# Kernel optimization log

Hardware: AMD Instinct MI355X
Metric: run time of the kernel (lower is better)

The kernel has to match this reference:

```python
import jax, jax.numpy as jnp
import numpy as np

B, T, D_IN, H1, H2 = 1024, 512, 128, 100, 100


def setup_inputs() -> dict:
    key = jax.random.key(0)
    ks = jax.random.split(key, 9)
    s1 = 1.0 / np.sqrt(H1)  # PyTorch LSTMCell init scale
    s2 = 1.0 / np.sqrt(H2)
    return {
        "x": jax.random.normal(ks[0], (B, T, D_IN), dtype=jnp.float32),
        "W_ih1": jax.random.normal(ks[1], (4 * H1, D_IN), dtype=jnp.float32) * s1,
        "W_hh1": jax.random.normal(ks[2], (4 * H1, H1), dtype=jnp.float32) * s1,
        "b_ih1": jax.random.normal(ks[3], (4 * H1,), dtype=jnp.float32) * s1,
        "b_hh1": jax.random.normal(ks[4], (4 * H1,), dtype=jnp.float32) * s1,
        "W_ih2": jax.random.normal(ks[5], (4 * H2, H1), dtype=jnp.float32) * s2,
        "W_hh2": jax.random.normal(ks[6], (4 * H2, H2), dtype=jnp.float32) * s2,
        "b_ih2": jax.random.normal(ks[7], (4 * H2,), dtype=jnp.float32) * s2,
        "b_hh2": jax.random.normal(ks[8], (4 * H2,), dtype=jnp.float32) * s2,
    }


def _lstm_cell(xt, h, c, W_ih, W_hh, b_ih, b_hh, H):
    # PyTorch LSTMCell: gates = x@W_ih^T + b_ih + h@W_hh^T + b_hh, chunked i,f,g,o
    gates = xt @ W_ih.T + h @ W_hh.T + (b_ih + b_hh)
    i = jax.nn.sigmoid(gates[:, 0 * H:1 * H])
    f = jax.nn.sigmoid(gates[:, 1 * H:2 * H])
    g = jnp.tanh(gates[:, 2 * H:3 * H])
    o = jax.nn.sigmoid(gates[:, 3 * H:4 * H])
    c_new = f * c + i * g
    h_new = o * jnp.tanh(c_new)
    return h_new, c_new


def reference(x, W_ih1, W_hh1, b_ih1, b_hh1, W_ih2, W_hh2, b_ih2, b_hh2):
    Bsz = x.shape[0]
    h1 = jnp.zeros((Bsz, H1), x.dtype)
    c1 = jnp.zeros((Bsz, H1), x.dtype)
    h2 = jnp.zeros((Bsz, H2), x.dtype)
    c2 = jnp.zeros((Bsz, H2), x.dtype)

    def step(carry, xt):
        h1, c1, h2, c2 = carry
        h1, c1 = _lstm_cell(xt, h1, c1, W_ih1, W_hh1, b_ih1, b_hh1, H1)
        # dropout(0.25) between layers: identity in eval mode (deterministic baseline)
        h2, c2 = _lstm_cell(h1, h2, c2, W_ih2, W_hh2, b_ih2, b_hh2, H2)
        return (h1, c1, h2, c2), h2

    xs = jnp.swapaxes(x, 0, 1)  # [T, B, D]
    _, ys = jax.lax.scan(step, (h1, c1, h2, c2), xs)
    return jnp.swapaxes(ys, 0, 1)  # [B, T, H2]
```

## Files before the change

kernel.cpp:

```cpp
#include <hip/hip_runtime.h>

#define B_TOT 1024
#define T_LEN 512
#define D_INP 128
#define H 100
#define HP 112
#define HX 128
#define NP 448
#define NT_TILES 28
#define FRAG_ELEMS 57344

#define LOG2E  1.4426950408889634f
#define LOG2E2 2.8853900817779268f

typedef _Float16 half8 __attribute__((ext_vector_type(8)));
typedef _Float16 half4 __attribute__((ext_vector_type(4)));
typedef float f32x4 __attribute__((ext_vector_type(4)));

#if __has_builtin(__builtin_amdgcn_exp2f)
__device__ __forceinline__ float EXP2(float x) { return __builtin_amdgcn_exp2f(x); }
#else
__device__ __forceinline__ float EXP2(float x) { return __expf(x * 0.6931471805599453f); }
#endif
#if __has_builtin(__builtin_amdgcn_rcpf)
__device__ __forceinline__ float RCP(float x) { return __builtin_amdgcn_rcpf(x); }
#else
__device__ __forceinline__ float RCP(float x) { return 1.0f / x; }
#endif

__device__ __forceinline__ float sig2(float zp)  { return RCP(1.0f + EXP2(-zp)); }
__device__ __forceinline__ float tanh2(float zp) { return 1.0f - 2.0f * RCP(EXP2(zp) + 1.0f); }
__device__ __forceinline__ float tanhc(float c)  { return 1.0f - 2.0f * RCP(EXP2(c * LOG2E2) + 1.0f); }
__device__ __forceinline__ float fast_sigmoid(float z) { return RCP(1.0f + EXP2(-z * LOG2E)); }
__device__ __forceinline__ float fast_tanh(float z)    { return 1.0f - 2.0f * RCP(EXP2(z * LOG2E2) + 1.0f); }

__device__ __forceinline__ unsigned pack2(float x, float y) {
    _Float16 a = (_Float16)x, b = (_Float16)y;
    unsigned short ua = __builtin_bit_cast(unsigned short, a);
    unsigned short ub = __builtin_bit_cast(unsigned short, b);
    return (unsigned)ua | ((unsigned)ub << 16);
}
__device__ __forceinline__ unsigned swz(int row, int colbyte) {
    return ((unsigned)row * 256u + (unsigned)colbyte) ^ (unsigned)((row & 7) << 4);
}
__device__ __forceinline__ void step_barrier() {
    asm volatile("s_waitcnt lgkmcnt(0)\n\ts_barrier" ::: "memory");
}

__global__ void init_states(float* s, int n) {
    int i = blockIdx.x * 256 + threadIdx.x;
    if (i < n) s[i] = 0.f;
}

__global__ void prep_frags(const float* __restrict__ Wih1, const float* __restrict__ Wih2,
                           const float* __restrict__ Whh1, const float* __restrict__ Whh2,
                           const float* __restrict__ bih1, const float* __restrict__ bhh1,
                           const float* __restrict__ bih2, const float* __restrict__ bhh2,
                           _Float16* __restrict__ frags, float* __restrict__ biases)
{
    int i = blockIdx.x * 256 + threadIdx.x;
    if (i < 4 * FRAG_ELEMS) {
        int sec = i / FRAG_ELEMS, j = i % FRAG_ELEMS;
        int e = j & 7, lane = (j >> 3) & 63, kt = (j >> 9) & 3, nt = j >> 11;
        int l = lane & 15, jb = nt >> 2, g = nt & 3;
        int hcol = jb * 16 + l;
        int k = kt * 32 + (lane >> 4) * 8 + e;
        const float* W = (sec == 0) ? Wih1 : (sec == 1) ? Wih2 : (sec == 2) ? Whh1 : Whh2;
        int Kreal = (sec == 0) ? 128 : 100;
        float v = 0.f;
        if (hcol < 100 && k < Kreal)
            v = W[(g * 100 + hcol) * Kreal + k] * ((g == 2) ? LOG2E2 : LOG2E);
        frags[i] = (_Float16)v;
        return;
    }
    i -= 4 * FRAG_ELEMS;
    if (i < 2 * NP) {
        int layer = i / NP, cp = i % NP;
        int jb = cp >> 6, g = (cp >> 4) & 3, l = cp & 15;
        int hcol = jb * 16 + l;
        float v = 0.f;
        if (hcol < 100) {
            int G = g * 100 + hcol;
            v = (layer ? (bih2[G] + bhh2[G]) : (bih1[G] + bhh1[G]))
              * ((g == 2) ? LOG2E2 : LOG2E);
        }
        biases[i] = v;
    }
}

template<int CT>
__global__ __launch_bounds__(512, 2) void superstep(
    const float* __restrict__ x,
    const _Float16* __restrict__ wfrag1, const float* __restrict__ bias1,
    _Float16* __restrict__ X1w, const _Float16* __restrict__ X1r,
    const _Float16* __restrict__ whhf1, _Float16* __restrict__ h1w,
    _Float16* __restrict__ hst1, float* __restrict__ cst1,
    const _Float16* __restrict__ h1r,
    const _Float16* __restrict__ wihf2, const _Float16* __restrict__ whhf2,
    const float* __restrict__ bias2p,
    _Float16* __restrict__ hst2, float* __restrict__ cst2,
    float* __restrict__ out,
    int t0g, int r1on, int t0r2)
{
    constexpr int LOG2CT = (CT == 128) ? 7 : (CT == 64) ? 6 : 5;
    __shared__ __align__(16) unsigned char smem[65536 + 2048];
    const int tid = threadIdx.x;
    const int blk = blockIdx.x;

    if (blk < 64) {
        if (!r1on) return;
        unsigned char* hr0 = smem;
        unsigned char* hr1 = smem + 4096;
        const int w = tid >> 6, lane = tid & 63;
        const bool active = w < 7;
        const int jb = w, l = lane & 15, rg = lane >> 4;
        const int bg = blk, b0 = bg * 16;
        const int col = jb * 16 + l;

        unsigned rdo[4], wro[4];
        #pragma unroll
        for (int kt = 0; kt < 4; ++kt) rdo[kt] = swz(l, (kt * 32 + rg * 8) * 2);
        #pragma unroll
        for (int r = 0; r < 4; ++r) wro[r] = swz(rg * 4 + r, col * 2);

        half8 bf[4][4];
        float cst[4];
        half4 xP[4];
        const _Float16* x_p = nullptr;
        _Float16* hs_p = nullptr;
        if (active) {
            #pragma unroll
            for (int g = 0; g < 4; ++g)
                #pragma unroll
                for (int kt = 0; kt < 4; ++kt)
                    bf[g][kt] = *reinterpret_cast<const half8*>(
                        whhf1 + (((long)(jb * 4 + g) * 4 + kt) * 64 + lane) * 8);
            x_p = X1r + (size_t)bg * CT * 16 * NP + (size_t)(rg * 4) * NP + jb * 64 + l * 4;
            hs_p = h1w + (size_t)bg * CT * 16 * HX + (size_t)(rg * 4) * HX + col;
            #pragma unroll
            for (int r = 0; r < 4; ++r) {
                cst[r] = cst1[(size_t)(b0 + rg * 4 + r) * HP + col];
                xP[r] = *reinterpret_cast<const half4*>(x_p + (size_t)r * NP);
            }
            x_p += (size_t)16 * NP;
        }
        if (tid < 64) {
            int buf = tid >> 5, r2i = (tid & 31) >> 1, c8 = 112 + (tid & 1) * 8;
            *reinterpret_cast<uint4*>((buf ? hr1 : hr0) + swz(r2i, c8 * 2)) = make_uint4(0u, 0u, 0u, 0u);
        }
        if (tid >= 64 && tid < 288) {
            int i = tid - 64, row = i / 14, c8 = (i % 14) * 8;
            *reinterpret_cast<uint4*>(hr1 + swz(row, c8 * 2)) =
                *reinterpret_cast<const uint4*>(hst1 + (size_t)(b0 + row) * HP + c8);
        }
        __syncthreads();

        auto STEP1 = [&](int it, const unsigned char* rb, unsigned char* wb)
            __attribute__((always_inline)) {
            half8 af[4];
            #pragma unroll
            for (int kt = 0; kt < 4; ++kt)
                af[kt] = *reinterpret_cast<const half8*>(rb + rdo[kt]);
            f32x4 acc[4];
            #pragma unroll
            for (int g = 0; g < 4; ++g)
                #pragma unroll
                for (int r = 0; r < 4; ++r) acc[g][r] = (float)xP[r][g];
            if (it + 1 < CT) {
                #pragma unroll
                for (int r = 0; r < 4; ++r)
                    xP[r] = *reinterpret_cast<const half4*>(x_p + (size_t)r * NP);
                x_p += (size_t)16 * NP;
            }
            #pragma unroll
            for (int kt = 0; kt < 4; ++kt)
                #pragma unroll
                for (int g = 0; g < 4; ++g)
                    acc[g] = __builtin_amdgcn_mfma_f32_16x16x32_f16(af[kt], bf[g][kt], acc[g], 0, 0, 0);
            #pragma unroll
            for (int r = 0; r < 4; ++r) {
                float ig = sig2(acc[0][r]);
                float fg = sig2(acc[1][r]);
                float gg = tanh2(acc[2][r]);
                float og = sig2(acc[3][r]);
                float c = fg * cst[r] + ig * gg;
                cst[r] = c;
                float h = og * tanhc(c);
                _Float16 hf = (_Float16)h;
                *reinterpret_cast<_Float16*>(wb + wro[r]) = hf;
                *(hs_p + (size_t)r * HX) = hf;
            }
            hs_p += (size_t)16 * HX;
        };

        for (int it = 0; it < CT; it += 2) {
            if (active) STEP1(it, hr1, hr0);
            step_barrier();
            if (active) STEP1(it + 1, hr0, hr1);
            step_barrier();
        }

        if (active) {
            #pragma unroll
            for (int r = 0; r < 4; ++r)
                cst1[(size_t)(b0 + rg * 4 + r) * HP + col] = cst[r];
        }
        if (tid < 224) {
            int row = tid / 14, c8 = (tid % 14) * 8;
            const unsigned char* sbuf = ((CT - 1) & 1) ? hr1 : hr0;
            *reinterpret_cast<uint4*>(hst1 + (size_t)(b0 + row) * HP + c8) =
                *reinterpret_cast<const uint4*>(sbuf + swz(row, c8 * 2));
        }
        return;
    }

    if (blk < 128) {
        if (t0r2 < 0) return;
        unsigned char* hr0 = smem;
        unsigned char* hr1 = smem + 4096;
        const int w = tid >> 6, lane = tid & 63;
        const bool active = w < 7;
        const int jb = w, l = lane & 15, rg = lane >> 4;
        const int bg = blk - 64, b0 = bg * 16;
        const int col = jb * 16 + l;

        unsigned rdo[4], wro[4];
        #pragma unroll
        for (int kt = 0; kt < 4; ++kt) rdo[kt] = swz(l, (kt * 32 + rg * 8) * 2);
        #pragma unroll
        for (int r = 0; r < 4; ++r) wro[r] = swz(rg * 4 + r, col * 2);

        half8 bi[4][4], bh[4][4];
        float b2v[4];
        float cst[4];
        half8 hP[4];
        const _Float16* hb_p = nullptr;
        float* out_p = nullptr;
        if (active) {
            #pragma unroll
            for (int g = 0; g < 4; ++g)
                #pragma unroll
                for (int kt = 0; kt < 4; ++kt) {
                    long o = (((long)(jb * 4 + g) * 4 + kt) * 64 + lane) * 8;
                    bi[g][kt] = *reinterpret_cast<const half8*>(wihf2 + o);
                    bh[g][kt] = *reinterpret_cast<const half8*>(whhf2 + o);
                }
            #pragma unroll
            for (int g = 0; g < 4; ++g) b2v[g] = bias2p[jb * 64 + g * 16 + l];
            hb_p = h1r + (size_t)bg * CT * 16 * HX + (size_t)l * HX + rg * 8;
            out_p = out + ((size_t)(b0 + rg * 4) * T_LEN + t0r2) * H + col;
            #pragma unroll
            for (int r = 0; r < 4; ++r)
                cst[r] = cst2[(size_t)(b0 + rg * 4 + r) * HP + col];
            #pragma unroll
            for (int kt = 0; kt < 4; ++kt)
                hP[kt] = *reinterpret_cast<const half8*>(hb_p + kt * 32);
        }
        if (tid < 64) {
            int buf = tid >> 5, r2i = (tid & 31) >> 1, c8 = 112 + (tid & 1) * 8;
            *reinterpret_cast<uint4*>((buf ? hr1 : hr0) + swz(r2i, c8 * 2)) = make_uint4(0u, 0u, 0u, 0u);
        }
        if (tid >= 64 && tid < 288) {
            int i = tid - 64, row = i / 14, c8 = (i % 14) * 8;
            *reinterpret_cast<uint4*>(hr1 + swz(row, c8 * 2)) =
                *reinterpret_cast<const uint4*>(hst2 + (size_t)(b0 + row) * HP + c8);
        }
        __syncthreads();

        auto STEP2 = [&](int it, const unsigned char* rb, unsigned char* wb)
            __attribute__((always_inline)) {
            half8 af2[4];
            #pragma unroll
            for (int kt = 0; kt < 4; ++kt)
                af2[kt] = *reinterpret_cast<const half8*>(rb + rdo[kt]);
            f32x4 acc[4];
            #pragma unroll
            for (int g = 0; g < 4; ++g)
                acc[g] = (f32x4){b2v[g], b2v[g], b2v[g], b2v[g]};
            #pragma unroll
            for (int kt = 0; kt < 4; ++kt)
                #pragma unroll
                for (int g = 0; g < 4; ++g)
                    acc[g] = __builtin_amdgcn_mfma_f32_16x16x32_f16(hP[kt], bi[g][kt], acc[g], 0, 0, 0);
            if (it + 1 < CT) {
                hb_p += (size_t)16 * HX;
                #pragma unroll
                for (int kt = 0; kt < 4; ++kt)
                    hP[kt] = *reinterpret_cast<const half8*>(hb_p + kt * 32);
            }
            #pragma unroll
            for (int kt = 0; kt < 4; ++kt)
                #pragma unroll
                for (int g = 0; g < 4; ++g)
                    acc[g] = __builtin_amdgcn_mfma_f32_16x16x32_f16(af2[kt], bh[g][kt], acc[g], 0, 0, 0);
            #pragma unroll
            for (int r = 0; r < 4; ++r) {
                float ig = sig2(acc[0][r]);
                float fg = sig2(acc[1][r]);
                float gg = tanh2(acc[2][r]);
                float og = sig2(acc[3][r]);
                float c = fg * cst[r] + ig * gg;
                cst[r] = c;
                float h = og * tanhc(c);
                *reinterpret_cast<_Float16*>(wb + wro[r]) = (_Float16)h;
                if (col < H) *(out_p + (size_t)r * T_LEN * H) = h;
            }
            out_p += H;
        };

        for (int it = 0; it < CT; it += 2) {
            if (active) STEP2(it, hr1, hr0);
            step_barrier();
            if (active) STEP2(it + 1, hr0, hr1);
            step_barrier();
        }

        if (active) {
            #pragma unroll
            for (int r = 0; r < 4; ++r)
                cst2[(size_t)(b0 + rg * 4 + r) * HP + col] = cst[r];
        }
        if (tid < 224) {
            int row = tid / 14, c8 = (tid % 14) * 8;
            const unsigned char* sbuf = ((CT - 1) & 1) ? hr1 : hr0;
            *reinterpret_cast<uint4*>(hst2 + (size_t)(b0 + row) * HP + c8) =
                *reinterpret_cast<const uint4*>(sbuf + swz(row, c8 * 2));
        }
        return;
    }

    if (t0g < 0) return;
    {
        unsigned char* sA = smem;
        float* sBias = reinterpret_cast<float*>(smem + 65536);
        const long row0 = (long)(blk - 128) * 256;

        {
            const int r = tid >> 1, kh = (tid & 1) * 64;
            long rr = row0 + r;
            long b = rr >> LOG2CT; int tc = (int)(rr & (CT - 1));
            const float* src = x + (b * T_LEN + t0g + tc) * D_INP;
            #pragma unroll
            for (int i = 0; i < 16; ++i) {
                int k = kh + i * 4;
                float4 v = *reinterpret_cast<const float4*>(src + k);
                unsigned off = ((unsigned)r * 256u + (unsigned)k * 2u) ^ (unsigned)((r & 7) << 4);
                *reinterpret_cast<uint2*>(sA + off) = make_uint2(pack2(v.x, v.y), pack2(v.z, v.w));
            }
        }
        for (int i = tid; i < NP; i += 512) sBias[i] = bias1[i];
        __syncthreads();

        const int wv = tid >> 6, lane = tid & 63;
        const int lrow = lane & 15, lk = (lane >> 4) * 8;

        half8 aF[2][4];
        #pragma unroll
        for (int s = 0; s < 2; ++s)
            #pragma unroll
            for (int kt = 0; kt < 4; ++kt) {
                int rowL = wv * 32 + s * 16 + lrow;
                unsigned off = ((unsigned)rowL * 256u + (unsigned)(kt * 32 + lk) * 2u)
                             ^ (unsigned)((rowL & 7) << 4);
                aF[s][kt] = *reinterpret_cast<const half8*>(sA + off);
            }

        unsigned ob[2][4];
        #pragma unroll
        for (int s = 0; s < 2; ++s)
            #pragma unroll
            for (int r = 0; r < 4; ++r) {
                long rgl = row0 + wv * 32 + s * 16 + (lane >> 4) * 4 + r;
                long b = rgl >> LOG2CT; int tc = (int)(rgl & (CT - 1));
                ob[s][r] = (unsigned)((((b >> 4) * CT + tc) * 16 + (b & 15)) * NP);
            }

        for (int nt = 0; nt < NT_TILES; ++nt) {
            half8 bF[4];
            const _Float16* bp = wfrag1 + ((long)(nt * 4) * 64 + lane) * 8;
            #pragma unroll
            for (int kt = 0; kt < 4; ++kt)
                bF[kt] = *reinterpret_cast<const half8*>(bp + (long)kt * 512);

            f32x4 acc0 = {0.f, 0.f, 0.f, 0.f}, acc1 = {0.f, 0.f, 0.f, 0.f};
            #pragma unroll
            for (int kt = 0; kt < 4; ++kt) {
                acc0 = __builtin_amdgcn_mfma_f32_16x16x32_f16(aF[0][kt], bF[kt], acc0, 0, 0, 0);
                acc1 = __builtin_amdgcn_mfma_f32_16x16x32_f16(aF[1][kt], bF[kt], acc1, 0, 0, 0);
            }
            const int col = nt * 16 + lrow;
            const int pcol = (col & ~63) | ((col & 15) << 2) | ((col >> 4) & 3);
            const float bv = sBias[col];
            #pragma unroll
            for (int r = 0; r < 4; ++r) {
                X1w[ob[0][r] + pcol] = (_Float16)(acc0[r] + bv);
                X1w[ob[1][r] + pcol] = (_Float16)(acc1[r] + bv);
            }
        }
    }
}

__global__ __launch_bounds__(256) void lstm2_persistent(
    const float* __restrict__ x,
    const float* __restrict__ W_ih1, const float* __restrict__ W_hh1,
    const float* __restrict__ b_ih1, const float* __restrict__ b_hh1,
    const float* __restrict__ W_ih2, const float* __restrict__ W_hh2,
    const float* __restrict__ b_ih2, const float* __restrict__ b_hh2,
    float* __restrict__ out)
{
    __shared__ float s_x[4][D_INP];
    __shared__ float s_h1[4][H], s_c1[4][H], s_h2[4][H], s_c2[4][H];
    __shared__ float s_g[4][400];
    __shared__ float s_b1[400], s_b2[400];
    const int tid = threadIdx.x;
    const int row0 = blockIdx.x * 4;
    for (int i = tid; i < 400; i += 256) { s_b1[i] = b_ih1[i] + b_hh1[i]; s_b2[i] = b_ih2[i] + b_hh2[i]; }
    for (int i = tid; i < 4 * H; i += 256) { int r = i / H, jj = i % H;
        s_h1[r][jj] = 0.f; s_c1[r][jj] = 0.f; s_h2[r][jj] = 0.f; s_c2[r][jj] = 0.f; }
    __syncthreads();
    for (int t = 0; t < T_LEN; ++t) {
        for (int i = tid; i < 4 * D_INP; i += 256) { int r = i >> 7, d = i & 127;
            s_x[r][d] = x[((size_t)(row0 + r) * T_LEN + t) * D_INP + d]; }
        __syncthreads();
        for (int g = tid; g < 400; g += 256) {
            float a0, a1, a2, a3; a0 = a1 = a2 = a3 = s_b1[g];
            const float4* wi = reinterpret_cast<const float4*>(W_ih1 + (size_t)g * D_INP);
            for (int d4 = 0; d4 < D_INP / 4; ++d4) {
                float4 wv = wi[d4];
                float4 v0 = *reinterpret_cast<const float4*>(&s_x[0][d4 * 4]);
                float4 v1 = *reinterpret_cast<const float4*>(&s_x[1][d4 * 4]);
                float4 v2 = *reinterpret_cast<const float4*>(&s_x[2][d4 * 4]);
                float4 v3 = *reinterpret_cast<const float4*>(&s_x[3][d4 * 4]);
                a0 += wv.x*v0.x + wv.y*v0.y + wv.z*v0.z + wv.w*v0.w;
                a1 += wv.x*v1.x + wv.y*v1.y + wv.z*v1.z + wv.w*v1.w;
                a2 += wv.x*v2.x + wv.y*v2.y + wv.z*v2.z + wv.w*v2.w;
                a3 += wv.x*v3.x + wv.y*v3.y + wv.z*v3.z + wv.w*v3.w;
            }
            const float4* wh = reinterpret_cast<const float4*>(W_hh1 + (size_t)g * H);
            for (int k4 = 0; k4 < H / 4; ++k4) {
                float4 wv = wh[k4];
                float4 v0 = *reinterpret_cast<const float4*>(&s_h1[0][k4 * 4]);
                float4 v1 = *reinterpret_cast<const float4*>(&s_h1[1][k4 * 4]);
                float4 v2 = *reinterpret_cast<const float4*>(&s_h1[2][k4 * 4]);
                float4 v3 = *reinterpret_cast<const float4*>(&s_h1[3][k4 * 4]);
                a0 += wv.x*v0.x + wv.y*v0.y + wv.z*v0.z + wv.w*v0.w;
                a1 += wv.x*v1.x + wv.y*v1.y + wv.z*v1.z + wv.w*v1.w;
                a2 += wv.x*v2.x + wv.y*v2.y + wv.z*v2.z + wv.w*v2.w;
                a3 += wv.x*v3.x + wv.y*v3.y + wv.z*v3.z + wv.w*v3.w;
            }
            s_g[0][g] = a0; s_g[1][g] = a1; s_g[2][g] = a2; s_g[3][g] = a3;
        }
        __syncthreads();
        for (int idx = tid; idx < 4 * H; idx += 256) {
            int r = idx / H, jj = idx % H;
            float ig = fast_sigmoid(s_g[r][jj]);
            float fg = fast_sigmoid(s_g[r][H + jj]);
            float gg = fast_tanh(s_g[r][2 * H + jj]);
            float og = fast_sigmoid(s_g[r][3 * H + jj]);
            float cc = fg * s_c1[r][jj] + ig * gg;
            s_c1[r][jj] = cc; s_h1[r][jj] = og * fast_tanh(cc);
        }
        __syncthreads();
        for (int g = tid; g < 400; g += 256) {
            float a0, a1, a2, a3; a0 = a1 = a2 = a3 = s_b2[g];
            const float4* wi = reinterpret_cast<const float4*>(W_ih2 + (size_t)g * H);
            const float4* wh = reinterpret_cast<const float4*>(W_hh2 + (size_t)g * H);
            for (int k4 = 0; k4 < H / 4; ++k4) {
                float4 wv = wi[k4];
                float4 v0 = *reinterpret_cast<const float4*>(&s_h1[0][k4 * 4]);
                float4 v1 = *reinterpret_cast<const float4*>(&s_h1[1][k4 * 4]);
                float4 v2 = *reinterpret_cast<const float4*>(&s_h1[2][k4 * 4]);
                float4 v3 = *reinterpret_cast<const float4*>(&s_h1[3][k4 * 4]);
                a0 += wv.x*v0.x + wv.y*v0.y + wv.z*v0.z + wv.w*v0.w;
                a1 += wv.x*v1.x + wv.y*v1.y + wv.z*v1.z + wv.w*v1.w;
                a2 += wv.x*v2.x + wv.y*v2.y + wv.z*v2.z + wv.w*v2.w;
                a3 += wv.x*v3.x + wv.y*v3.y + wv.z*v3.z + wv.w*v3.w;
            }
            for (int k4 = 0; k4 < H / 4; ++k4) {
                float4 wv = wh[k4];
                float4 v0 = *reinterpret_cast<const float4*>(&s_h2[0][k4 * 4]);
                float4 v1 = *reinterpret_cast<const float4*>(&s_h2[1][k4 * 4]);
                float4 v2 = *reinterpret_cast<const float4*>(&s_h2[2][k4 * 4]);
                float4 v3 = *reinterpret_cast<const float4*>(&s_h2[3][k4 * 4]);
                a0 += wv.x*v0.x + wv.y*v0.y + wv.z*v0.z + wv.w*v0.w;
                a1 += wv.x*v1.x + wv.y*v1.y + wv.z*v1.z + wv.w*v1.w;
                a2 += wv.x*v2.x + wv.y*v2.y + wv.z*v2.z + wv.w*v2.w;
                a3 += wv.x*v3.x + wv.y*v3.y + wv.z*v3.z + wv.w*v3.w;
            }
            s_g[0][g] = a0; s_g[1][g] = a1; s_g[2][g] = a2; s_g[3][g] = a3;
        }
        __syncthreads();
        for (int idx = tid; idx < 4 * H; idx += 256) {
            int r = idx / H, jj = idx % H;
            float ig = fast_sigmoid(s_g[r][jj]);
            float fg = fast_sigmoid(s_g[r][H + jj]);
            float gg = fast_tanh(s_g[r][2 * H + jj]);
            float og = fast_sigmoid(s_g[r][3 * H + jj]);
            float cc = fg * s_c2[r][jj] + ig * gg;
            s_c2[r][jj] = cc;
            float hn = og * fast_tanh(cc);
            s_h2[r][jj] = hn;
            out[((size_t)(row0 + r) * T_LEN + t) * H + jj] = hn;
        }
        __syncthreads();
    }
}

template<int CT>
static void run_pipeline(const float* x, float* out,
                         _Float16* X1a, _Float16* X1b, _Float16* h1a, _Float16* h1b,
                         float* cst1, float* cst2, _Float16* hst1, _Float16* hst2,
                         const _Float16* wfrag1, const _Float16* wihf2,
                         const _Float16* whhf1, const _Float16* whhf2,
                         const float* bias1, const float* bias2,
                         hipStream_t stream)
{
    const int nCh = T_LEN / CT;
    const unsigned grid = 128u + (unsigned)((size_t)B_TOT * CT / 256);
    for (int k = 0; k <= nCh + 1; ++k) {
        int t0g  = (k < nCh) ? k * CT : -1;
        int r1on = (k >= 1 && k <= nCh) ? 1 : 0;
        int t0r2 = (k >= 2) ? (k - 2) * CT : -1;
        _Float16* X1w = (k & 1) ? X1b : X1a;
        const _Float16* X1r = (k & 1) ? X1a : X1b;
        _Float16* h1w = (k & 1) ? h1a : h1b;
        const _Float16* h1r = (k & 1) ? h1b : h1a;
        superstep<CT><<<grid, 512, 0, stream>>>(
            x, wfrag1, bias1, X1w, X1r,
            whhf1, h1w, hst1, cst1,
            h1r, wihf2, whhf2, bias2, hst2, cst2, out,
            t0g, r1on, t0r2);
    }
}

extern "C" void kernel_launch(void* const* d_in, const int* in_sizes, int n_in,
                              void* d_out, int out_size, void* d_ws, size_t ws_size,
                              hipStream_t stream) {
    const float* x     = (const float*)d_in[0];
    const float* W_ih1 = (const float*)d_in[1];
    const float* W_hh1 = (const float*)d_in[2];
    const float* b_ih1 = (const float*)d_in[3];
    const float* b_hh1 = (const float*)d_in[4];
    const float* W_ih2 = (const float*)d_in[5];
    const float* W_hh2 = (const float*)d_in[6];
    const float* b_ih2 = (const float*)d_in[7];
    const float* b_hh2 = (const float*)d_in[8];
    float* out = (float*)d_out;

    auto need = [](int CT) -> size_t {
        return 2ull * B_TOT * CT * NP * 2
             + 2ull * B_TOT * CT * HX * 2
             + 2ull * B_TOT * HP * 4
             + 2ull * B_TOT * HP * 2
             + 4ull * FRAG_ELEMS * 2
             + 2ull * NP * 4
             + 256;
    };

    int CT = 0;
    if (ws_size >= need(32)) CT = 32;
    else if (ws_size >= need(64)) CT = 64;

    if (CT == 0) {
        lstm2_persistent<<<B_TOT / 4, 256, 0, stream>>>(
            x, W_ih1, W_hh1, b_ih1, b_hh1, W_ih2, W_hh2, b_ih2, b_hh2, out);
        return;
    }

    char* p = (char*)d_ws;
    size_t xchunk = (size_t)B_TOT * (size_t)CT;
    _Float16* X1a = (_Float16*)p;     p += xchunk * NP * 2;
    _Float16* X1b = (_Float16*)p;     p += xchunk * NP * 2;
    _Float16* h1a = (_Float16*)p;     p += xchunk * HX * 2;
    _Float16* h1b = (_Float16*)p;     p += xchunk * HX * 2;
    float* cst1 = (float*)p;          p += (size_t)B_TOT * HP * 4;
    float* cst2 = (float*)p;          p += (size_t)B_TOT * HP * 4;
    _Float16* hst1 = (_Float16*)p;    p += (size_t)B_TOT * HP * 2;
    _Float16* hst2 = (_Float16*)p;    p += (size_t)B_TOT * HP * 2;
    _Float16* frags = (_Float16*)p;   p += 4ull * FRAG_ELEMS * 2;
    float* biases = (float*)p;        p += 2ull * NP * 4;

    const _Float16* wfrag1 = frags;
    const _Float16* wihf2  = frags + FRAG_ELEMS;
    const _Float16* whhf1  = frags + 2ull * FRAG_ELEMS;
    const _Float16* whhf2  = frags + 3ull * FRAG_ELEMS;
    const float* bias1 = biases;
    const float* bias2 = biases + NP;

    int nzero = 3 * B_TOT * HP;
    init_states<<<(nzero + 255) / 256, 256, 0, stream>>>(cst1, nzero);

    int nprep = 4 * FRAG_ELEMS + 2 * NP;
    prep_frags<<<(nprep + 255) / 256, 256, 0, stream>>>(
        W_ih1, W_ih2, W_hh1, W_hh2, b_ih1, b_hh1, b_ih2, b_hh2, frags, biases);

    if (CT == 32)
        run_pipeline<32>(x, out, X1a, X1b, h1a, h1b, cst1, cst2, hst1, hst2,
                         wfrag1, wihf2, whhf1, whhf2, bias1, bias2, stream);
    else
        run_pipeline<64>(x, out, X1a, X1b, h1a, h1b, cst1, cst2, hst1, hst2,
                         wfrag1, wihf2, whhf1, whhf2, bias1, bias2, stream);
}
```

Measured before the change: 799.9 us.

## Fuse layer-1 input projection into recurrent step, drop precompute GEMM stage

Removes the separate pipeline stage that precomputed the layer-1 input projection into a half-precision workspace buffer. The layer-1 recurrent blocks now load raw x rows each step, pack them to fp16 and run extra MFMAs against resident W_ih1 fragments, starting the accumulator from the bias. This cuts the pipeline from three stages to two, trims the grid to 128 blocks, shrinks shared memory and prefers a larger chunk size. In exchange it adds per-step MFMA work and global x loads to the latency-critical recurrent loop, and doubles the weight registers held per lane.

```diff
diff --git a/kernel.cpp b/kernel.cpp
--- a/kernel.cpp
+++ b/kernel.cpp
@@ -7,14 +7,12 @@
 #define HP 112
 #define HX 128
 #define NP 448
-#define NT_TILES 28
 #define FRAG_ELEMS 57344
 
 #define LOG2E  1.4426950408889634f
 #define LOG2E2 2.8853900817779268f
 
 typedef _Float16 half8 __attribute__((ext_vector_type(8)));
-typedef _Float16 half4 __attribute__((ext_vector_type(4)));
 typedef float f32x4 __attribute__((ext_vector_type(4)));
 
 #if __has_builtin(__builtin_amdgcn_exp2f)
@@ -39,6 +37,10 @@
     unsigned short ua = __builtin_bit_cast(unsigned short, a);
     unsigned short ub = __builtin_bit_cast(unsigned short, b);
     return (unsigned)ua | ((unsigned)ub << 16);
+}
+__device__ __forceinline__ half8 pack8(float4 a, float4 b) {
+    uint4 v = make_uint4(pack2(a.x, a.y), pack2(a.z, a.w), pack2(b.x, b.y), pack2(b.z, b.w));
+    return __builtin_bit_cast(half8, v);
 }
 __device__ __forceinline__ unsigned swz(int row, int colbyte) {
     return ((unsigned)row * 256u + (unsigned)colbyte) ^ (unsigned)((row & 7) << 4);
@@ -91,58 +93,66 @@
 template<int CT>
 __global__ __launch_bounds__(512, 2) void superstep(
     const float* __restrict__ x,
-    const _Float16* __restrict__ wfrag1, const float* __restrict__ bias1,
-    _Float16* __restrict__ X1w, const _Float16* __restrict__ X1r,
-    const _Float16* __restrict__ whhf1, _Float16* __restrict__ h1w,
+    const _Float16* __restrict__ wihf1, const _Float16* __restrict__ whhf1,
+    const float* __restrict__ bias1p,
+    _Float16* __restrict__ h1w,
     _Float16* __restrict__ hst1, float* __restrict__ cst1,
     const _Float16* __restrict__ h1r,
     const _Float16* __restrict__ wihf2, const _Float16* __restrict__ whhf2,
     const float* __restrict__ bias2p,
     _Float16* __restrict__ hst2, float* __restrict__ cst2,
     float* __restrict__ out,
-    int t0g, int r1on, int t0r2)
+    int t0r1, int t0r2)
 {
-    constexpr int LOG2CT = (CT == 128) ? 7 : (CT == 64) ? 6 : 5;
-    __shared__ __align__(16) unsigned char smem[65536 + 2048];
+    __shared__ __align__(16) unsigned char smem[8192];
     const int tid = threadIdx.x;
     const int blk = blockIdx.x;
 
+    unsigned char* hr0 = smem;
+    unsigned char* hr1 = smem + 4096;
+    const int w = tid >> 6, lane = tid & 63;
+    const bool active = w < 7;
+    const int jb = w, l = lane & 15, rg = lane >> 4;
+    const int col = jb * 16 + l;
+
+    unsigned rdo[4], wro[4];
+    #pragma unroll
+    for (int kt = 0; kt < 4; ++kt) rdo[kt] = swz(l, (kt * 32 + rg * 8) * 2);
+    #pragma unroll
+    for (int r = 0; r < 4; ++r) wro[r] = swz(rg * 4 + r, col * 2);
+
     if (blk < 64) {
-        if (!r1on) return;
-        unsigned char* hr0 = smem;
-        unsigned char* hr1 = smem + 4096;
-        const int w = tid >> 6, lane = tid & 63;
-        const bool active = w < 7;
-        const int jb = w, l = lane & 15, rg = lane >> 4;
+        if (t0r1 < 0) return;
         const int bg = blk, b0 = bg * 16;
-        const int col = jb * 16 + l;
-
-        unsigned rdo[4], wro[4];
-        #pragma unroll
-        for (int kt = 0; kt < 4; ++kt) rdo[kt] = swz(l, (kt * 32 + rg * 8) * 2);
-        #pragma unroll
-        for (int r = 0; r < 4; ++r) wro[r] = swz(rg * 4 + r, col * 2);
-
-        half8 bf[4][4];
+
+        half8 bi[4][4], bf[4][4];
+        float b1v[4];
         float cst[4];
-        half4 xP[4];
-        const _Float16* x_p = nullptr;
+        float4 xr[4][2];
+        const float* xg_p = nullptr;
         _Float16* hs_p = nullptr;
         if (active) {
             #pragma unroll
             for (int g = 0; g < 4; ++g)
                 #pragma unroll
-                for (int kt = 0; kt < 4; ++kt)
-                    bf[g][kt] = *reinterpret_cast<const half8*>(
-                        whhf1 + (((long)(jb * 4 + g) * 4 + kt) * 64 + lane) * 8);
-            x_p = X1r + (size_t)bg * CT * 16 * NP + (size_t)(rg * 4) * NP + jb * 64 + l * 4;
+                for (int kt = 0; kt < 4; ++kt) {
+                    long o = (((long)(jb * 4 + g) * 4 + kt) * 64 + lane) * 8;
+                    bi[g][kt] = *reinterpret_cast<const half8*>(wihf1 + o);
+                    bf[g][kt] = *reinterpret_cast<const half8*>(whhf1 + o);
+                }
+            #pragma unroll
+            for (int g = 0; g < 4; ++g) b1v[g] = bias1p[jb * 64 + g * 16 + l];
+            xg_p = x + ((size_t)(b0 + l) * T_LEN + t0r1) * D_INP + rg * 8;
             hs_p = h1w + (size_t)bg * CT * 16 * HX + (size_t)(rg * 4) * HX + col;
             #pragma unroll
-            for (int r = 0; r < 4; ++r) {
+            for (int r = 0; r < 4; ++r)
                 cst[r] = cst1[(size_t)(b0 + rg * 4 + r) * HP + col];
-                xP[r] = *reinterpret_cast<const half4*>(x_p + (size_t)r * NP);
-            }
-            x_p += (size_t)16 * NP;
+            #pragma unroll
+            for (int kt = 0; kt < 4; ++kt) {
+                xr[kt][0] = *reinterpret_cast<const float4*>(xg_p + kt * 32);
+                xr[kt][1] = *reinterpret_cast<const float4*>(xg_p + kt * 32 + 4);
+            }
+            xg_p += D_INP;
         }
         if (tid < 64) {
             int buf = tid >> 5, r2i = (tid & 31) >> 1, c8 = 112 + (tid & 1) * 8;
@@ -157,21 +167,29 @@
 
         auto STEP1 = [&](int it, const unsigned char* rb, unsigned char* wb)
             __attribute__((always_inline)) {
-            half8 af[4];
+            half8 af[4], ax[4];
+            #pragma unroll
+            for (int kt = 0; kt < 4; ++kt) {
+                af[kt] = *reinterpret_cast<const half8*>(rb + rdo[kt]);
+                ax[kt] = pack8(xr[kt][0], xr[kt][1]);
+            }
+            if (it + 1 < CT) {
+                #pragma unroll
+                for (int kt = 0; kt < 4; ++kt) {
+                    xr[kt][0] = *reinterpret_cast<const float4*>(xg_p + kt * 32);
+                    xr[kt][1] = *reinterpret_cast<const float4*>(xg_p + kt * 32 + 4);
+                }
+                xg_p += D_INP;
+            }
+            f32x4 acc[4];
+            #pragma unroll
+            for (int g = 0; g < 4; ++g)
+                acc[g] = (f32x4){b1v[g], b1v[g], b1v[g], b1v[g]};
             #pragma unroll
             for (int kt = 0; kt < 4; ++kt)
-                af[kt] = *reinterpret_cast<const half8*>(rb + rdo[kt]);
-            f32x4 acc[4];
-            #pragma unroll
-            for (int g = 0; g < 4; ++g)
-                #pragma unroll
-                for (int r = 0; r < 4; ++r) acc[g][r] = (float)xP[r][g];
-            if (it + 1 < CT) {
-                #pragma unroll
-                for (int r = 0; r < 4; ++r)
-                    xP[r] = *reinterpret_cast<const half4*>(x_p + (size_t)r * NP);
-                x_p += (size_t)16 * NP;
-            }
+                #pragma unroll
+                for (int g = 0; g < 4; ++g)
+                    acc[g] = __builtin_amdgcn_mfma_f32_16x16x32_f16(ax[kt], bi[g][kt], acc[g], 0, 0, 0);
             #pragma unroll
             for (int kt = 0; kt < 4; ++kt)
                 #pragma unroll
@@ -214,21 +232,9 @@
         return;
     }
 
-    if (blk < 128) {
+    {
         if (t0r2 < 0) return;
-        unsigned char* hr0 = smem;
-        unsigned char* hr1 = smem + 4096;
-        const int w = tid >> 6, lane = tid & 63;
-        const bool active = w < 7;
-        const int jb = w, l = lane & 15, rg = lane >> 4;
         const int bg = blk - 64, b0 = bg * 16;
-        const int col = jb * 16 + l;
-
-        unsigned rdo[4], wro[4];
-        #pragma unroll
-        for (int kt = 0; kt < 4; ++kt) rdo[kt] = swz(l, (kt * 32 + rg * 8) * 2);
-        #pragma unroll
-        for (int r = 0; r < 4; ++r) wro[r] = swz(rg * 4 + r, col * 2);
 
         half8 bi[4][4], bh[4][4];
         float b2v[4];
@@ -325,77 +331,6 @@
             const unsigned char* sbuf = ((CT - 1) & 1) ? hr1 : hr0;
             *reinterpret_cast<uint4*>(hst2 + (size_t)(b0 + row) * HP + c8) =
                 *reinterpret_cast<const uint4*>(sbuf + swz(row, c8 * 2));
-        }
-        return;
-    }
-
-    if (t0g < 0) return;
-    {
-        unsigned char* sA = smem;
-        float* sBias = reinterpret_cast<float*>(smem + 65536);
-        const long row0 = (long)(blk - 128) * 256;
-
-        {
-            const int r = tid >> 1, kh = (tid & 1) * 64;
-            long rr = row0 + r;
-            long b = rr >> LOG2CT; int tc = (int)(rr & (CT - 1));
-            const float* src = x + (b * T_LEN + t0g + tc) * D_INP;
-            #pragma unroll
-            for (int i = 0; i < 16; ++i) {
-                int k = kh + i * 4;
-                float4 v = *reinterpret_cast<const float4*>(src + k);
-                unsigned off = ((unsigned)r * 256u + (unsigned)k * 2u) ^ (unsigned)((r & 7) << 4);
-                *reinterpret_cast<uint2*>(sA + off) = make_uint2(pack2(v.x, v.y), pack2(v.z, v.w));
-            }
-        }
-        for (int i = tid; i < NP; i += 512) sBias[i] = bias1[i];
-        __syncthreads();
-
-        const int wv = tid >> 6, lane = tid & 63;
-        const int lrow = lane & 15, lk = (lane >> 4) * 8;
-
-        half8 aF[2][4];
-        #pragma unroll
-        for (int s = 0; s < 2; ++s)
-            #pragma unroll
-            for (int kt = 0; kt < 4; ++kt) {
-                int rowL = wv * 32 + s * 16 + lrow;
-                unsigned off = ((unsigned)rowL * 256u + (unsigned)(kt * 32 + lk) * 2u)
-                             ^ (unsigned)((rowL & 7) << 4);
-                aF[s][kt] = *reinterpret_cast<const half8*>(sA + off);
-            }
-
-        unsigned ob[2][4];
-        #pragma unroll
-        for (int s = 0; s < 2; ++s)
-            #pragma unroll
-            for (int r = 0; r < 4; ++r) {
-                long rgl = row0 + wv * 32 + s * 16 + (lane >> 4) * 4 + r;
-                long b = rgl >> LOG2CT; int tc = (int)(rgl & (CT - 1));
-                ob[s][r] = (unsigned)((((b >> 4) * CT + tc) * 16 + (b & 15)) * NP);
-            }
-
-        for (int nt = 0; nt < NT_TILES; ++nt) {
-            half8 bF[4];
-            const _Float16* bp = wfrag1 + ((long)(nt * 4) * 64 + lane) * 8;
-            #pragma unroll
-            for (int kt = 0; kt < 4; ++kt)
-                bF[kt] = *reinterpret_cast<const half8*>(bp + (long)kt * 512);
-
-            f32x4 acc0 = {0.f, 0.f, 0.f, 0.f}, acc1 = {0.f, 0.f, 0.f, 0.f};
-            #pragma unroll
-            for (int kt = 0; kt < 4; ++kt) {
-                acc0 = __builtin_amdgcn_mfma_f32_16x16x32_f16(aF[0][kt], bF[kt], acc0, 0, 0, 0);
-                acc1 = __builtin_amdgcn_mfma_f32_16x16x32_f16(aF[1][kt], bF[kt], acc1, 0, 0, 0);
-            }
-            const int col = nt * 16 + lrow;
-            const int pcol = (col & ~63) | ((col & 15) << 2) | ((col >> 4) & 3);
-            const float bv = sBias[col];
-            #pragma unroll
-            for (int r = 0; r < 4; ++r) {
-                X1w[ob[0][r] + pcol] = (_Float16)(acc0[r] + bv);
-                X1w[ob[1][r] + pcol] = (_Float16)(acc1[r] + bv);
-            }
         }
     }
 }
@@ -508,28 +443,23 @@
 
 template<int CT>
 static void run_pipeline(const float* x, float* out,
-                         _Float16* X1a, _Float16* X1b, _Float16* h1a, _Float16* h1b,
+                         _Float16* h1a, _Float16* h1b,
                          float* cst1, float* cst2, _Float16* hst1, _Float16* hst2,
-                         const _Float16* wfrag1, const _Float16* wihf2,
+                         const _Float16* wihf1, const _Float16* wihf2,
                          const _Float16* whhf1, const _Float16* whhf2,
                          const float* bias1, const float* bias2,
                          hipStream_t stream)
 {
     const int nCh = T_LEN / CT;
-    const unsigned grid = 128u + (unsigned)((size_t)B_TOT * CT / 256);
-    for (int k = 0; k <= nCh + 1; ++k) {
-        int t0g  = (k < nCh) ? k * CT : -1;
-        int r1on = (k >= 1 && k <= nCh) ? 1 : 0;
-        int t0r2 = (k >= 2) ? (k - 2) * CT : -1;
-        _Float16* X1w = (k & 1) ? X1b : X1a;
-        const _Float16* X1r = (k & 1) ? X1a : X1b;
-        _Float16* h1w = (k & 1) ? h1a : h1b;
-        const _Float16* h1r = (k & 1) ? h1b : h1a;
-        superstep<CT><<<grid, 512, 0, stream>>>(
-            x, wfrag1, bias1, X1w, X1r,
-            whhf1, h1w, hst1, cst1,
+    for (int k = 0; k <= nCh; ++k) {
+        int t0r1 = (k < nCh) ? k * CT : -1;
+        int t0r2 = (k >= 1) ? (k - 1) * CT : -1;
+        _Float16* h1w = (k & 1) ? h1b : h1a;
+        const _Float16* h1r = (k & 1) ? h1a : h1b;
+        superstep<CT><<<128, 512, 0, stream>>>(
+            x, wihf1, whhf1, bias1, h1w, hst1, cst1,
             h1r, wihf2, whhf2, bias2, hst2, cst2, out,
-            t0g, r1on, t0r2);
+            t0r1, t0r2);
     }
 }
 
@@ -548,8 +478,7 @@
     float* out = (float*)d_out;
 
     auto need = [](int CT) -> size_t {
-        return 2ull * B_TOT * CT * NP * 2
-             + 2ull * B_TOT * CT * HX * 2
+        return 2ull * B_TOT * CT * HX * 2
              + 2ull * B_TOT * HP * 4
              + 2ull * B_TOT * HP * 2
              + 4ull * FRAG_ELEMS * 2
@@ -558,8 +487,8 @@
     };
 
     int CT = 0;
-    if (ws_size >= need(32)) CT = 32;
-    else if (ws_size >= need(64)) CT = 64;
+    if (ws_size >= need(64)) CT = 64;
+    else if (ws_size >= need(32)) CT = 32;
 
     if (CT == 0) {
         lstm2_persistent<<<B_TOT / 4, 256, 0, stream>>>(
@@ -569,8 +498,6 @@
 
     char* p = (char*)d_ws;
     size_t xchunk = (size_t)B_TOT * (size_t)CT;
-    _Float16* X1a = (_Float16*)p;     p += xchunk * NP * 2;
-    _Float16* X1b = (_Float16*)p;     p += xchunk * NP * 2;
     _Float16* h1a = (_Float16*)p;     p += xchunk * HX * 2;
     _Float16* h1b = (_Float16*)p;     p += xchunk * HX * 2;
     float* cst1 = (float*)p;          p += (size_t)B_TOT * HP * 4;
@@ -580,10 +507,10 @@
     _Float16* frags = (_Float16*)p;   p += 4ull * FRAG_ELEMS * 2;
     float* biases = (float*)p;        p += 2ull * NP * 4;
 
-    const _Float16* wfrag1 = frags;
-    const _Float16* wihf2  = frags + FRAG_ELEMS;
-    const _Float16* whhf1  = frags + 2ull * FRAG_ELEMS;
-    const _Float16* whhf2  = frags + 3ull * FRAG_ELEMS;
+    const _Float16* wihf1 = frags;
+    const _Float16* wihf2 = frags + FRAG_ELEMS;
+    const _Float16* whhf1 = frags + 2ull * FRAG_ELEMS;
+    const _Float16* whhf2 = frags + 3ull * FRAG_ELEMS;
     const float* bias1 = biases;
     const float* bias2 = biases + NP;
 
@@ -594,10 +521,10 @@
     prep_frags<<<(nprep + 255) / 256, 256, 0, stream>>>(
         W_ih1, W_ih2, W_hh1, W_hh2, b_ih1, b_hh1, b_ih2, b_hh2, frags, biases);
 
-    if (CT == 32)
-        run_pipeline<32>(x, out, X1a, X1b, h1a, h1b, cst1, cst2, hst1, hst2,
-                         wfrag1, wihf2, whhf1, whhf2, bias1, bias2, stream);
+    if (CT == 64)
+        run_pipeline<64>(x, out, h1a, h1b, cst1, cst2, hst1, hst2,
+                         wihf1, wihf2, whhf1, whhf2, bias1, bias2, stream);
     else
-        run_pipeline<64>(x, out, X1a, X1b, h1a, h1b, cst1, cst2, hst1, hst2,
-                         wfrag1, wihf2, whhf1, whhf2, bias1, bias2, stream);
-}
+        run_pipeline<32>(x, out, h1a, h1b, cst1, cst2, hst1, hst2,
+                         wihf1, wihf2, whhf1, whhf2, bias1, bias2, stream);
+}
```

After: 1.371 ms. 71.4% more time.
